# Kernel tuning notes

Hardware: AMD Instinct MI355X
Metric: run time of the kernel (lower is better)

The kernel has to match this reference:

```python
import jax, jax.numpy as jnp
import numpy as np

NH, DH = 16, 64          # n_head, d_head
CH = NH + DH             # 80
RQ, RK, RV = 6, 2, 2
ROPE_BASE = 10000.0


def _rotary(b, cache_len):
    # b: [B, T, R, DH]; rotates the d-factor exactly as the torch Rotary module
    T = b.shape[1]
    inv_freq = (1.0 / ROPE_BASE) ** (jnp.arange(0, DH, 2, dtype=jnp.float32) / DH)
    t = jnp.arange(T, dtype=jnp.float32) + cache_len
    freqs = jnp.outer(t, inv_freq)                      # [T, DH/2]
    cos = freqs[None, :, None, :].astype(b.dtype)
    sin = jnp.sin(freqs)[None, :, None, :].astype(b.dtype)
    cos = jnp.cos(freqs)[None, :, None, :].astype(b.dtype)
    x1, x2 = jnp.split(b, 2, axis=3)
    return jnp.concatenate([x1 * cos + x2 * sin, -x1 * sin + x2 * cos], axis=3)


def setup_inputs() -> dict:
    key = jax.random.key(0)
    k1, k2, k3, k4 = jax.random.split(key, 4)
    B, T, D = 2, 2048, 1024
    x = jax.random.normal(k1, (B, T, D), dtype=jnp.float32)
    # xavier-uniform-like scale for factor projections
    s_q = float(np.sqrt(6.0 / (D + CH)))
    s_o = float(np.sqrt(6.0 / (D + D)))
    W_abq = jax.random.uniform(k2, (RQ * CH, D), minval=-s_q, maxval=s_q, dtype=jnp.float32)
    W_abkv = jax.random.uniform(k3, ((RK + RV) * CH, D), minval=-s_q, maxval=s_q, dtype=jnp.float32)
    W_o = jax.random.uniform(k4, (D, D), minval=-s_o, maxval=s_o, dtype=jnp.float32)
    return {"x": x, "W_abq": W_abq, "W_abkv": W_abkv, "W_o": W_o}


def reference(x, W_abq, W_abkv, W_o):
    B, T, D = x.shape
    # low-rank factor projections
    abq = (x @ W_abq.T).reshape(B, T, RQ, CH)
    a_q, b_q = abq[..., :NH], abq[..., NH:]            # [B,T,RQ,NH], [B,T,RQ,DH]
    abkv = (x @ W_abkv.T).reshape(B, T, RK + RV, CH)
    a_kv = abkv[..., :NH]
    b_kv = _rotary(abkv[..., NH:], cache_len=0)        # RoPE applied to K/V d-factors only
    a_k, b_k = a_kv[:, :, :RK], b_kv[:, :, :RK]
    a_v, b_v = a_kv[:, :, RK:], b_kv[:, :, RK:]
    # tensor-product reconstruction of Q/K/V
    q = jnp.einsum('btrh,btrd->bthd', a_q, b_q) / RQ
    k = jnp.einsum('btrh,btrd->bthd', a_k, b_k) / RK
    v = jnp.einsum('btrh,btrd->bthd', a_v, b_v) / RV
    # causal attention (flex_attention default scale = 1/sqrt(dh))
    scale = 1.0 / jnp.sqrt(jnp.asarray(DH, dtype=q.dtype))
    scores = jnp.einsum('bqhd,bkhd->bhqk', q, k) * scale
    causal = jnp.tril(jnp.ones((T, T), dtype=bool))
    scores = jnp.where(causal[None, None], scores, jnp.finfo(scores.dtype).min)
    attn = jax.nn.softmax(scores, axis=-1)
    y = jnp.einsum('bhqk,bkhd->bqhd', attn, v).reshape(B, T, D)
    return y @ W_o.T
```

## Files before the change

kernel.cpp:

```cpp
#include <hip/hip_runtime.h>
#include <hip/hip_bf16.h>
#include <math.h>

#define NHEADS 16
#define DHEAD  64
#define CHDIM  80
#define RQn    6
#define RKn    2
#define RVn    2
#define BB     2
#define TT     2048
#define DDim   1024
#define NQK    800

using frag16 = __attribute__((ext_vector_type(8))) short;
using f32x4  = __attribute__((ext_vector_type(4))) float;
using f32x16 = __attribute__((ext_vector_type(16))) float;
using uint2v = __attribute__((ext_vector_type(2))) unsigned int;

#define AS1(p) ((const __attribute__((address_space(1))) unsigned int*)(p))
#define AS3(p) ((__attribute__((address_space(3))) unsigned int*)(p))

static __device__ __forceinline__ unsigned short bf16_bits(float f) {
    __hip_bfloat16 h = __float2bfloat16(f);
    return *(unsigned short*)&h;
}
static __device__ __forceinline__ unsigned int pk2(float a, float b) {
    return ((unsigned int)bf16_bits(b) << 16) | (unsigned int)bf16_bits(a);
}
static __device__ __forceinline__ float bfu2f(unsigned short u) {
    return __uint_as_float(((unsigned int)u) << 16);
}
static __device__ __forceinline__ float exp2_hw(float x) {
    return __builtin_amdgcn_exp2f(x);
}

__global__ __launch_bounds__(256) void cvt_all(
    const float* __restrict__ x, const float* __restrict__ wq,
    const float* __restrict__ wk, const float* __restrict__ wo,
    __hip_bfloat16* __restrict__ xb, __hip_bfloat16* __restrict__ wqk,
    __hip_bfloat16* __restrict__ wob)
{
    int bid = blockIdx.x;
    const float* src; __hip_bfloat16* dst; int n4;
    if (bid < 4096)      { src = x;  dst = xb;            n4 = 1048576; }
    else if (bid < 4576) { bid -= 4096; src = wq; dst = wqk;           n4 = 122880; }
    else if (bid < 4896) { bid -= 4576; src = wk; dst = wqk + 491520;  n4 = 81920; }
    else                 { bid -= 4896; src = wo; dst = wob;           n4 = 262144; }
    int i = bid * 256 + threadIdx.x;
    if (i < n4) {
        float4 v = *(const float4*)&src[i * 4];
        ushort4 o;
        o.x = bf16_bits(v.x); o.y = bf16_bits(v.y);
        o.z = bf16_bits(v.z); o.w = bf16_bits(v.w);
        *(ushort4*)&dst[i * 4] = o;
    }
}

template <bool BF16OUT>
__global__ __launch_bounds__(256) void gemm_bf16(
    const __hip_bfloat16* __restrict__ A, const __hip_bfloat16* __restrict__ W,
    void* __restrict__ Cv, int M, int N, int K)
{
    __shared__ __hip_bfloat16 Asl[2][64 * 64];
    __shared__ __hip_bfloat16 Bsl[2][128 * 64];
    const int tid = threadIdx.x;
    const int w = tid >> 6, lane = tid & 63;
    const int l16 = lane & 15, quad = lane >> 4;
    const int bm = blockIdx.y * 64, bn = blockIdx.x * 128;

    int rSA[2], cSA[2];
    #pragma unroll
    for (int j = 0; j < 2; j++) {
        int L = (w * 2 + j) * 64 + lane;
        rSA[j] = L >> 3;
        cSA[j] = (L & 7) ^ (rSA[j] & 7);
    }
    int rSB[4], cSB[4];
    #pragma unroll
    for (int j = 0; j < 4; j++) {
        int L = (w * 4 + j) * 64 + lane;
        int r = L >> 3;
        cSB[j] = (L & 7) ^ (r & 7);
        int rb = bn + r;
        rSB[j] = (rb < N) ? rb : (N - 1);
    }

    f32x4 acc[4][2];
    #pragma unroll
    for (int mt = 0; mt < 4; mt++)
        #pragma unroll
        for (int nt = 0; nt < 2; nt++)
            acc[mt][nt] = (f32x4){0.f, 0.f, 0.f, 0.f};

    const int nK = K >> 6;
    #pragma unroll
    for (int j = 0; j < 2; j++)
        __builtin_amdgcn_global_load_lds(AS1(A + (size_t)(bm + rSA[j]) * K + cSA[j] * 8),
                                         AS3(&Asl[0][(w * 2 + j) * 512]), 16, 0, 0);
    #pragma unroll
    for (int j = 0; j < 4; j++)
        __builtin_amdgcn_global_load_lds(AS1(W + (size_t)rSB[j] * K + cSB[j] * 8),
                                         AS3(&Bsl[0][(w * 4 + j) * 512]), 16, 0, 0);

    for (int kk = 0; kk < nK; kk++) {
        const int cur = kk & 1;
        __syncthreads();
        if (kk + 1 < nK) {
            const int k1 = (kk + 1) * 64;
            #pragma unroll
            for (int j = 0; j < 2; j++)
                __builtin_amdgcn_global_load_lds(AS1(A + (size_t)(bm + rSA[j]) * K + k1 + cSA[j] * 8),
                                                 AS3(&Asl[cur ^ 1][(w * 2 + j) * 512]), 16, 0, 0);
            #pragma unroll
            for (int j = 0; j < 4; j++)
                __builtin_amdgcn_global_load_lds(AS1(W + (size_t)rSB[j] * K + k1 + cSB[j] * 8),
                                                 AS3(&Bsl[cur ^ 1][(w * 4 + j) * 512]), 16, 0, 0);
        }
        #pragma unroll
        for (int ks = 0; ks < 2; ks++) {
            frag16 af[4], bf[2];
            #pragma unroll
            for (int mt = 0; mt < 4; mt++) {
                int r = mt * 16 + l16;
                af[mt] = *(const frag16*)&Asl[cur][r * 64 + (((ks * 4 + quad) ^ (r & 7)) * 8)];
            }
            #pragma unroll
            for (int nt = 0; nt < 2; nt++) {
                int r = w * 32 + nt * 16 + l16;
                bf[nt] = *(const frag16*)&Bsl[cur][r * 64 + (((ks * 4 + quad) ^ (r & 7)) * 8)];
            }
            #pragma unroll
            for (int mt = 0; mt < 4; mt++)
                #pragma unroll
                for (int nt = 0; nt < 2; nt++)
                    acc[mt][nt] = __builtin_amdgcn_mfma_f32_16x16x32_bf16(af[mt], bf[nt], acc[mt][nt], 0, 0, 0);
        }
    }
    #pragma unroll
    for (int mt = 0; mt < 4; mt++) {
        #pragma unroll
        for (int reg = 0; reg < 4; reg++) {
            int row = bm + mt * 16 + quad * 4 + reg;
            #pragma unroll
            for (int nt = 0; nt < 2; nt++) {
                int col = bn + w * 32 + nt * 16 + l16;
                if (col < N) {
                    if constexpr (BF16OUT)
                        ((__hip_bfloat16*)Cv)[(size_t)row * N + col] = __float2bfloat16(acc[mt][nt][reg]);
                    else
                        ((float*)Cv)[(size_t)row * N + col] = acc[mt][nt][reg];
                }
            }
        }
    }
}

__global__ __launch_bounds__(256) void qkv_kernel(
    const __hip_bfloat16* __restrict__ ab,
    __hip_bfloat16* __restrict__ q, __hip_bfloat16* __restrict__ k,
    __hip_bfloat16* __restrict__ vT)
{
    const int tok0 = blockIdx.x * 4;
    const int w = threadIdx.x >> 6;
    const int d = threadIdx.x & 63;
    const int token = tok0 + w;
    const int b = token / TT;
    const int t = token % TT;
    __shared__ float sab[4][NQK];
    __shared__ __align__(8) __hip_bfloat16 vbuf[NHEADS][DHEAD][4];
    const __hip_bfloat16* aq = ab + (size_t)token * NQK;
    #pragma unroll
    for (int i2 = d; i2 < NQK / 2; i2 += 64) {
        unsigned int u = *(const unsigned int*)&aq[i2 * 2];
        sab[w][i2 * 2 + 0] = bfu2f((unsigned short)(u & 0xffff));
        sab[w][i2 * 2 + 1] = bfu2f((unsigned short)(u >> 16));
    }
    const float* sq  = sab[w];
    const float* skv = sab[w] + 480;
    const int i32 = d & 31;
    float inv_freq = exp2_hw(-(float)i32 * (13.287712379549449f / 32.0f));
    float fr = (float)t * inv_freq;
    float c = cosf(fr), s = sinf(fr);
    __syncthreads();
    float rot[4];
    #pragma unroll
    for (int r = 0; r < 4; r++) {
        float x1 = skv[r * CHDIM + NHEADS + i32];
        float x2 = skv[r * CHDIM + NHEADS + 32 + i32];
        rot[r] = (d < 32) ? (x1 * c + x2 * s) : (-x1 * s + x2 * c);
    }
    float bqv[RQn];
    #pragma unroll
    for (int r = 0; r < RQn; r++) bqv[r] = sq[r * CHDIM + NHEADS + d];
    #pragma unroll
    for (int h = 0; h < NHEADS; h++) {
        float accq = 0.0f;
        #pragma unroll
        for (int r = 0; r < RQn; r++)
            accq += sq[r * CHDIM + h] * bqv[r];
        q[((size_t)(b * NHEADS + h) * TT + t) * DHEAD + d] =
            __float2bfloat16(accq * (0.125f / 6.0f) * 1.4426950408889634f);
        float acck = 0.0f, accv = 0.0f;
        #pragma unroll
        for (int r = 0; r < RKn; r++)
            acck += skv[r * CHDIM + h] * rot[r];
        #pragma unroll
        for (int r = 0; r < RVn; r++)
            accv += skv[(RKn + r) * CHDIM + h] * rot[RKn + r];
        k[((size_t)(b * NHEADS + h) * TT + t) * DHEAD + d] = __float2bfloat16(acck * 0.5f);
        vbuf[h][d][w] = __float2bfloat16(accv * 0.5f);
    }
    __syncthreads();
    const int t0 = tok0 % TT;
    const int b0 = tok0 / TT;
    for (int row = threadIdx.x; row < NHEADS * DHEAD; row += 256) {
        int h = row >> 6, dd = row & 63;
        *(uint2*)&vT[((size_t)(b0 * NHEADS + h) * DHEAD + dd) * TT + t0] =
            *(const uint2*)&vbuf[h][dd][0];
    }
}

static __device__ __forceinline__ void build_pfrag(
    const float* s0, const float* s1, frag16 Pf[4])
{
    #pragma unroll
    for (int k2 = 0; k2 < 4; k2++) {
        const float* sF = (k2 >= 2) ? s1 : s0;
        const int bs = 8 * (k2 & 1);
        unsigned int a0 = pk2(sF[bs + 0], sF[bs + 1]);
        unsigned int b0 = pk2(sF[bs + 2], sF[bs + 3]);
        unsigned int a1 = pk2(sF[bs + 4], sF[bs + 5]);
        unsigned int b1 = pk2(sF[bs + 6], sF[bs + 7]);
        uint2v ra = __builtin_amdgcn_permlane32_swap(a0, a1, false, false);
        uint2v rb = __builtin_amdgcn_permlane32_swap(b0, b1, false, false);
        union { frag16 f; unsigned int u[4]; } pf;
        pf.u[0] = ra[0]; pf.u[1] = rb[0]; pf.u[2] = ra[1]; pf.u[3] = rb[1];
        Pf[k2] = pf.f;
    }
}

static __device__ __forceinline__ void attn_tile(
    const __hip_bfloat16* __restrict__ Kc, const __hip_bfloat16* __restrict__ Vc,
    const frag16 qB[4], f32x16& O0, f32x16& O1, float& lpart,
    const int l31, const int hi, const int xi,
    const bool domask, const int kb0, const int qlane)
{
    f32x16 ST0 = {}, ST1 = {};
    __builtin_amdgcn_s_setprio(1);
    #pragma unroll
    for (int kt4 = 0; kt4 < 4; kt4++) {
        int c8 = kt4 * 2 + hi;
        frag16 kf0 = *(const frag16*)&Kc[l31 * 64 + ((c8 ^ xi) * 8)];
        frag16 kf1 = *(const frag16*)&Kc[(32 + l31) * 64 + ((c8 ^ xi) * 8)];
        ST0 = __builtin_amdgcn_mfma_f32_32x32x16_bf16(kf0, qB[kt4], ST0, 0, 0, 0);
        ST1 = __builtin_amdgcn_mfma_f32_32x32x16_bf16(kf1, qB[kt4], ST1, 0, 0, 0);
    }
    __builtin_amdgcn_s_setprio(0);
    float* s0 = (float*)&ST0;
    float* s1 = (float*)&ST1;
    if (domask) {
        int kbq = kb0 + 4 * hi;
        #pragma unroll
        for (int reg = 0; reg < 16; reg++) {
            int rowc = (reg & 3) + 8 * (reg >> 2);
            if (kbq + rowc > qlane)      s0[reg] = -1e30f;
            if (kbq + 32 + rowc > qlane) s1[reg] = -1e30f;
        }
    }
    #pragma unroll
    for (int reg = 0; reg < 16; reg++) {
        float p0 = exp2_hw(s0[reg]);
        float p1 = exp2_hw(s1[reg]);
        s0[reg] = p0; s1[reg] = p1;
        lpart += p0 + p1;
    }
    frag16 Pf[4];
    build_pfrag(s0, s1, Pf);
    __builtin_amdgcn_s_setprio(1);
    #pragma unroll
    for (int k2 = 0; k2 < 4; k2++) {
        int c8 = k2 * 2 + hi;
        frag16 vf0 = *(const frag16*)&Vc[l31 * 64 + ((c8 ^ xi) * 8)];
        frag16 vf1 = *(const frag16*)&Vc[(32 + l31) * 64 + ((c8 ^ xi) * 8)];
        O0 = __builtin_amdgcn_mfma_f32_32x32x16_bf16(vf0, Pf[k2], O0, 0, 0, 0);
        O1 = __builtin_amdgcn_mfma_f32_32x32x16_bf16(vf1, Pf[k2], O1, 0, 0, 0);
    }
    __builtin_amdgcn_s_setprio(0);
}

__global__ __launch_bounds__(512, 4) void flash_mfma(
    const __hip_bfloat16* __restrict__ q, const __hip_bfloat16* __restrict__ k,
    const __hip_bfloat16* __restrict__ vT, __hip_bfloat16* __restrict__ y)
{
    const int Bid = blockIdx.x;
    const int m = Bid & 255;
    const int half = Bid >> 8;
    const int xcd = m & 7;
    const int bh  = xcd * 4 + ((m >> 3) & 3);
    const int qx  = m >> 5;
    const int qt  = half ? qx : (15 - qx);
    const int nst = qt + 1;

    const int tid = threadIdx.x;
    const int w8 = tid >> 6;
    const int part = w8 >> 2;
    const int w = w8 & 3;
    const int lane = tid & 63;
    const int l31 = lane & 31;
    const int hi = lane >> 5;
    const int xi = l31 & 7;
    const int paddr = (lane ^ 32) << 2;
    const int k0 = part * nst;

    __shared__ __align__(16) char smem[65536];
    __hip_bfloat16* Ks = (__hip_bfloat16*)(smem + part * 32768);
    __hip_bfloat16* Vs = (__hip_bfloat16*)(smem + part * 32768 + 16384);

    const size_t base = (size_t)bh * TT * DHEAD;
    const __hip_bfloat16* qb = q + base;
    const __hip_bfloat16* kb = k + base;
    const __hip_bfloat16* vb = vT + base;

    const int ktd = 2 * qt + (w >> 1);
    const int qlane = qt * 128 + w * 32 + l31;

    int offK[2], offV[2];
    #pragma unroll
    for (int j = 0; j < 2; j++) {
        int Lc = w * 128 + j * 64 + lane;
        int r = Lc >> 3, c8 = Lc & 7, g8 = c8 ^ (r & 7);
        offK[j] = r * 64 + g8 * 8;
        offV[j] = r * TT + g8 * 8;
    }

    frag16 qB[4];
    #pragma unroll
    for (int kt4 = 0; kt4 < 4; kt4++)
        qB[kt4] = *(const frag16*)&qb[(size_t)qlane * DHEAD + kt4 * 16 + hi * 8];

    f32x16 O0 = {}, O1 = {};
    float l = 0.0f;

    #pragma unroll
    for (int j = 0; j < 2; j++) {
        __builtin_amdgcn_global_load_lds(AS1(kb + (size_t)k0 * 4096 + offK[j]),
                                         AS3(&Ks[w * 1024 + j * 512]), 16, 0, 0);
        __builtin_amdgcn_global_load_lds(AS1(vb + (size_t)k0 * 64 + offV[j]),
                                         AS3(&Vs[w * 1024 + j * 512]), 16, 0, 0);
    }

    for (int kt = 0; kt < nst; kt++) {
        const int cur = kt & 1;
        __syncthreads();
        if (kt + 1 < nst) {
            const int phys1 = k0 + kt + 1;
            #pragma unroll
            for (int j = 0; j < 2; j++) {
                __builtin_amdgcn_global_load_lds(AS1(kb + (size_t)phys1 * 4096 + offK[j]),
                                                 AS3(&Ks[(cur ^ 1) * 4096 + w * 1024 + j * 512]), 16, 0, 0);
                __builtin_amdgcn_global_load_lds(AS1(vb + (size_t)phys1 * 64 + offV[j]),
                                                 AS3(&Vs[(cur ^ 1) * 4096 + w * 1024 + j * 512]), 16, 0, 0);
            }
        }
        const int phys = k0 + kt;
        if (phys <= ktd)
            attn_tile(Ks + cur * 4096, Vs + cur * 4096, qB, O0, O1, l,
                      l31, hi, xi, phys == ktd, phys * 64, qlane);
    }

    __syncthreads();
    float* Oex = (float*)smem;
    float* lex = (float*)(smem + 33792);
    float* o0 = (float*)&O0;
    float* o1 = (float*)&O1;
    if (part == 1) {
        float* dst = Oex + (w * 64 + lane) * 33;
        #pragma unroll
        for (int i = 0; i < 16; i++) { dst[i] = o0[i]; dst[16 + i] = o1[i]; }
        lex[w * 64 + lane] = l;
    }
    __syncthreads();
    if (part == 0) {
        const float* src = Oex + (w * 64 + lane) * 33;
        #pragma unroll
        for (int i = 0; i < 16; i++) { o0[i] += src[i]; o1[i] += src[16 + i]; }
        l += lex[w * 64 + lane];
        float lother = __int_as_float(__builtin_amdgcn_ds_bpermute(paddr, __float_as_int(l)));
        float inv = 1.0f / (l + lother);
        const int b = bh >> 4, h = bh & 15;
        __hip_bfloat16* yp = y + ((size_t)(b * TT + qlane)) * DDim + h * DHEAD;
        #pragma unroll
        for (int gg = 0; gg < 4; gg++) {
            int d0 = 8 * gg + 4 * hi;
            uint2 pa, pb;
            pa.x = pk2(o0[4*gg+0] * inv, o0[4*gg+1] * inv);
            pa.y = pk2(o0[4*gg+2] * inv, o0[4*gg+3] * inv);
            pb.x = pk2(o1[4*gg+0] * inv, o1[4*gg+1] * inv);
            pb.y = pk2(o1[4*gg+2] * inv, o1[4*gg+3] * inv);
            *(uint2*)&yp[d0] = pa;
            *(uint2*)&yp[32 + d0] = pb;
        }
    }
}

extern "C" void kernel_launch(void* const* d_in, const int* in_sizes, int n_in,
                              void* d_out, int out_size, void* d_ws, size_t ws_size,
                              hipStream_t stream) {
    const float* x      = (const float*)d_in[0];
    const float* W_abq  = (const float*)d_in[1];
    const float* W_abkv = (const float*)d_in[2];
    const float* W_o    = (const float*)d_in[3];
    float* out = (float*)d_out;

    char* ws = (char*)d_ws;
    __hip_bfloat16* xb   = (__hip_bfloat16*)ws;  ws += (size_t)4194304 * 2;
    __hip_bfloat16* wqk  = (__hip_bfloat16*)ws;  ws += (size_t)NQK * 1024 * 2;
    __hip_bfloat16* wo_b = (__hip_bfloat16*)ws;  ws += (size_t)1048576 * 2;
    __hip_bfloat16* abqkv = (__hip_bfloat16*)ws; ws += (size_t)4096 * NQK * 2;
    __hip_bfloat16* qb = (__hip_bfloat16*)ws;    ws += (size_t)4194304 * 2;
    __hip_bfloat16* kb = (__hip_bfloat16*)ws;    ws += (size_t)4194304 * 2;
    __hip_bfloat16* vT = (__hip_bfloat16*)ws;    ws += (size_t)4194304 * 2;
    __hip_bfloat16* yb = (__hip_bfloat16*)ws;    ws += (size_t)4194304 * 2;

    cvt_all<<<dim3(5920), dim3(256), 0, stream>>>(x, W_abq, W_abkv, W_o, xb, wqk, wo_b);
    gemm_bf16<true><<<dim3(7, 64), dim3(256), 0, stream>>>(xb, wqk, abqkv, 4096, NQK, 1024);
    qkv_kernel<<<dim3(1024), dim3(256), 0, stream>>>(abqkv, qb, kb, vT);
    flash_mfma<<<dim3(512), dim3(512), 0, stream>>>(qb, kb, vT, yb);
    gemm_bf16<false><<<dim3(8, 64), dim3(256), 0, stream>>>(yb, wo_b, out, 4096, 1024, 1024);
}
```

Baseline: 157.8 us.

## Split flash attention into single-wave blocks with private K/V staging

The attention kernel goes from 512-thread blocks, where 8 waves shared cooperatively loaded K/V tiles and merged two key-range halves through LDS, to 2048 one-wave blocks. Each wave loads its own K/V tiles into double-buffered LDS and synchronises with vmcnt waits instead of block barriers. This removes __syncthreads and the cross-part reduction. In exchange, each wave issues 4x more global-to-LDS loads, K/V reuse across waves is lost, and the key-range split for load balancing is dropped, so long causal rows run serially on one wave.

```diff
diff --git a/kernel.cpp b/kernel.cpp
--- a/kernel.cpp
+++ b/kernel.cpp
@@ -289,33 +289,26 @@
     __builtin_amdgcn_s_setprio(0);
 }
 
-__global__ __launch_bounds__(512, 4) void flash_mfma(
+__global__ __launch_bounds__(64) void flash_mfma(
     const __hip_bfloat16* __restrict__ q, const __hip_bfloat16* __restrict__ k,
     const __hip_bfloat16* __restrict__ vT, __hip_bfloat16* __restrict__ y)
 {
     const int Bid = blockIdx.x;
-    const int m = Bid & 255;
-    const int half = Bid >> 8;
-    const int xcd = m & 7;
-    const int bh  = xcd * 4 + ((m >> 3) & 3);
-    const int qx  = m >> 5;
-    const int qt  = half ? qx : (15 - qx);
-    const int nst = qt + 1;
-
-    const int tid = threadIdx.x;
-    const int w8 = tid >> 6;
-    const int part = w8 >> 2;
-    const int w = w8 & 3;
-    const int lane = tid & 63;
+    const int xcd = Bid & 7;
+    const int bhsub = (Bid >> 3) & 3;
+    const int w = (Bid >> 5) & 3;
+    const int qtIdx = (Bid >> 7) & 15;
+    const int qt = 15 - qtIdx;
+    const int bh = xcd * 4 + bhsub;
+
+    const int lane = threadIdx.x;
     const int l31 = lane & 31;
     const int hi = lane >> 5;
     const int xi = l31 & 7;
     const int paddr = (lane ^ 32) << 2;
-    const int k0 = part * nst;
-
-    __shared__ __align__(16) char smem[65536];
-    __hip_bfloat16* Ks = (__hip_bfloat16*)(smem + part * 32768);
-    __hip_bfloat16* Vs = (__hip_bfloat16*)(smem + part * 32768 + 16384);
+
+    __shared__ __align__(16) __hip_bfloat16 Ks[2][4096];
+    __shared__ __align__(16) __hip_bfloat16 Vs[2][4096];
 
     const size_t base = (size_t)bh * TT * DHEAD;
     const __hip_bfloat16* qb = q + base;
@@ -323,13 +316,14 @@
     const __hip_bfloat16* vb = vT + base;
 
     const int ktd = 2 * qt + (w >> 1);
+    const int nsteps = ktd + 1;
     const int qlane = qt * 128 + w * 32 + l31;
 
-    int offK[2], offV[2];
-    #pragma unroll
-    for (int j = 0; j < 2; j++) {
-        int Lc = w * 128 + j * 64 + lane;
-        int r = Lc >> 3, c8 = Lc & 7, g8 = c8 ^ (r & 7);
+    int offK[8], offV[8];
+    #pragma unroll
+    for (int j = 0; j < 8; j++) {
+        int L = j * 64 + lane;
+        int r = L >> 3, c8 = L & 7, g8 = c8 ^ (r & 7);
         offK[j] = r * 64 + g8 * 8;
         offV[j] = r * TT + g8 * 8;
     }
@@ -338,69 +332,51 @@
     #pragma unroll
     for (int kt4 = 0; kt4 < 4; kt4++)
         qB[kt4] = *(const frag16*)&qb[(size_t)qlane * DHEAD + kt4 * 16 + hi * 8];
+    asm volatile("s_waitcnt vmcnt(0)" ::: "memory");
+
+#define STAGE_TILE(PHYS, BUF)                                                          \
+    _Pragma("unroll")                                                                  \
+    for (int j = 0; j < 8; j++) {                                                      \
+        __builtin_amdgcn_global_load_lds(AS1(kb + (size_t)(PHYS) * 4096 + offK[j]),    \
+                                         AS3(&Ks[BUF][j * 512]), 16, 0, 0);            \
+        __builtin_amdgcn_global_load_lds(AS1(vb + (size_t)(PHYS) * 64 + offV[j]),      \
+                                         AS3(&Vs[BUF][j * 512]), 16, 0, 0);            \
+    }
 
     f32x16 O0 = {}, O1 = {};
     float l = 0.0f;
 
-    #pragma unroll
-    for (int j = 0; j < 2; j++) {
-        __builtin_amdgcn_global_load_lds(AS1(kb + (size_t)k0 * 4096 + offK[j]),
-                                         AS3(&Ks[w * 1024 + j * 512]), 16, 0, 0);
-        __builtin_amdgcn_global_load_lds(AS1(vb + (size_t)k0 * 64 + offV[j]),
-                                         AS3(&Vs[w * 1024 + j * 512]), 16, 0, 0);
-    }
-
-    for (int kt = 0; kt < nst; kt++) {
-        const int cur = kt & 1;
-        __syncthreads();
-        if (kt + 1 < nst) {
-            const int phys1 = k0 + kt + 1;
-            #pragma unroll
-            for (int j = 0; j < 2; j++) {
-                __builtin_amdgcn_global_load_lds(AS1(kb + (size_t)phys1 * 4096 + offK[j]),
-                                                 AS3(&Ks[(cur ^ 1) * 4096 + w * 1024 + j * 512]), 16, 0, 0);
-                __builtin_amdgcn_global_load_lds(AS1(vb + (size_t)phys1 * 64 + offV[j]),
-                                                 AS3(&Vs[(cur ^ 1) * 4096 + w * 1024 + j * 512]), 16, 0, 0);
-            }
+    STAGE_TILE(0, 0);
+    for (int phys = 0; phys < nsteps; phys++) {
+        const int cur = phys & 1;
+        if (phys + 1 < nsteps) {
+            STAGE_TILE(phys + 1, cur ^ 1);
+            asm volatile("s_waitcnt vmcnt(16)" ::: "memory");
+        } else {
+            asm volatile("s_waitcnt vmcnt(0)" ::: "memory");
         }
-        const int phys = k0 + kt;
-        if (phys <= ktd)
-            attn_tile(Ks + cur * 4096, Vs + cur * 4096, qB, O0, O1, l,
-                      l31, hi, xi, phys == ktd, phys * 64, qlane);
-    }
-
-    __syncthreads();
-    float* Oex = (float*)smem;
-    float* lex = (float*)(smem + 33792);
+        __builtin_amdgcn_sched_barrier(0);
+        attn_tile(Ks[cur], Vs[cur], qB, O0, O1, l,
+                  l31, hi, xi, phys == ktd, phys * 64, qlane);
+    }
+#undef STAGE_TILE
+
+    float lother = __int_as_float(__builtin_amdgcn_ds_bpermute(paddr, __float_as_int(l)));
+    float inv = 1.0f / (l + lother);
     float* o0 = (float*)&O0;
     float* o1 = (float*)&O1;
-    if (part == 1) {
-        float* dst = Oex + (w * 64 + lane) * 33;
-        #pragma unroll
-        for (int i = 0; i < 16; i++) { dst[i] = o0[i]; dst[16 + i] = o1[i]; }
-        lex[w * 64 + lane] = l;
-    }
-    __syncthreads();
-    if (part == 0) {
-        const float* src = Oex + (w * 64 + lane) * 33;
-        #pragma unroll
-        for (int i = 0; i < 16; i++) { o0[i] += src[i]; o1[i] += src[16 + i]; }
-        l += lex[w * 64 + lane];
-        float lother = __int_as_float(__builtin_amdgcn_ds_bpermute(paddr, __float_as_int(l)));
-        float inv = 1.0f / (l + lother);
-        const int b = bh >> 4, h = bh & 15;
-        __hip_bfloat16* yp = y + ((size_t)(b * TT + qlane)) * DDim + h * DHEAD;
-        #pragma unroll
-        for (int gg = 0; gg < 4; gg++) {
-            int d0 = 8 * gg + 4 * hi;
-            uint2 pa, pb;
-            pa.x = pk2(o0[4*gg+0] * inv, o0[4*gg+1] * inv);
-            pa.y = pk2(o0[4*gg+2] * inv, o0[4*gg+3] * inv);
-            pb.x = pk2(o1[4*gg+0] * inv, o1[4*gg+1] * inv);
-            pb.y = pk2(o1[4*gg+2] * inv, o1[4*gg+3] * inv);
-            *(uint2*)&yp[d0] = pa;
-            *(uint2*)&yp[32 + d0] = pb;
-        }
+    const int b = bh >> 4, h = bh & 15;
+    __hip_bfloat16* yp = y + ((size_t)(b * TT + qlane)) * DDim + h * DHEAD;
+    #pragma unroll
+    for (int gg = 0; gg < 4; gg++) {
+        int d0 = 8 * gg + 4 * hi;
+        uint2 pa, pb;
+        pa.x = pk2(o0[4*gg+0] * inv, o0[4*gg+1] * inv);
+        pa.y = pk2(o0[4*gg+2] * inv, o0[4*gg+3] * inv);
+        pb.x = pk2(o1[4*gg+0] * inv, o1[4*gg+1] * inv);
+        pb.y = pk2(o1[4*gg+2] * inv, o1[4*gg+3] * inv);
+        *(uint2*)&yp[d0] = pa;
+        *(uint2*)&yp[32 + d0] = pb;
     }
 }
 
@@ -426,6 +402,6 @@
     cvt_all<<<dim3(5920), dim3(256), 0, stream>>>(x, W_abq, W_abkv, W_o, xb, wqk, wo_b);
     gemm_bf16<true><<<dim3(7, 64), dim3(256), 0, stream>>>(xb, wqk, abqkv, 4096, NQK, 1024);
     qkv_kernel<<<dim3(1024), dim3(256), 0, stream>>>(abqkv, qb, kb, vT);
-    flash_mfma<<<dim3(512), dim3(512), 0, stream>>>(qb, kb, vT, yb);
+    flash_mfma<<<dim3(2048), dim3(64), 0, stream>>>(qb, kb, vT, yb);
     gemm_bf16<false><<<dim3(8, 64), dim3(256), 0, stream>>>(yb, wo_b, out, 4096, 1024, 1024);
 }
```

Result: slower. 182.5 us (+15.6%).
